# Optimization experiments

Measured on AMD Instinct MI355X. Metric: run time of the kernel, lower is better.

## Reference

```python
import jax, jax.numpy as jnp
import numpy as np

B, T, R, NS = 16, 2048, 256, 4


def setup_inputs() -> dict:
    key = jax.random.key(0)
    ks = jax.random.split(key, 11)
    s = 1.0 / np.sqrt(R)
    inp = {
        "q": jax.random.normal(ks[0], (B, T, R), jnp.float32),
        "k": jax.random.normal(ks[1], (B, T, R), jnp.float32),
        "v": jax.random.normal(ks[2], (B, T, R), jnp.float32),
        "wq": jax.random.uniform(ks[3], (R, R), jnp.float32, -s, s),
        "bq": jax.random.uniform(ks[4], (R,), jnp.float32, -s, s),
        "wk": jax.random.uniform(ks[5], (R, R), jnp.float32, -s, s),
        "bk": jax.random.uniform(ks[6], (R,), jnp.float32, -s, s),
        "wv": jax.random.uniform(ks[7], (NS, R, R), jnp.float32, -s, s),
        "bv": jax.random.uniform(ks[8], (NS, R), jnp.float32, -s, s),
        "wp": jax.random.uniform(ks[9], (R,), jnp.float32, -s, s),
        "bp": jax.random.uniform(ks[10], (), jnp.float32, -s, s),
    }
    return inp


def reference(q, k, v, wq, bq, wk, bk, wv, bv, wp, bp):
    # linear projections (torch Linear: x @ W.T + b)
    qp = q @ wq.T + bq                                   # [B,T,R]
    kp = k @ wk.T + bk                                   # [B,T,R]
    # n_state value projections, stacked on dim 1 -> [B,NS,T,R]
    vs = jnp.einsum('btr,nor->bnto', v, wv) + bv[None, :, None, :]

    # scaled dot-product attention with tril + (score==0 -> -10000) mask quirk
    scale = 1.0 / jnp.sqrt(jnp.asarray(q.shape[-1], qp.dtype))
    score = jnp.einsum('btr,bsr->bts', qp, kp) * scale   # [B,T,T]
    score = jnp.tril(score)
    score = jnp.where(score == 0, jnp.asarray(-10000.0, score.dtype), score)
    attn = jax.nn.softmax(score, axis=-1)                # [B,T,T]

    # batched AV (original does a python loop over batch; same math)
    out = jnp.einsum('bts,bnsr->bntr', attn, vs)         # [B,NS,T,R]

    # similarity loss: 0.5 * sum |cov(proj_score[b])| averaged over batch
    proj = jnp.einsum('bntr,r->bnt', vs, wp) + bp        # [B,NS,T]

    def cov_abs_sum(X):  # X: [NS, T], rows = variables
        Xc = X - X.mean(axis=1, keepdims=True)
        c = (Xc @ Xc.T) / (X.shape[1] - 1)               # [NS,NS]
        return 0.5 * jnp.sum(jnp.abs(c))

    sim_loss = jnp.mean(jax.vmap(cov_abs_sum)(proj))
    return out, sim_loss
```

## Files before the change

### kernel.cpp

```cpp
#include <hip/hip_runtime.h>

#define B_  16
#define T_  2048
#define R_  256
#define NS_ 4

typedef unsigned short u16;
typedef __attribute__((ext_vector_type(8))) __bf16 bf16x8;
typedef __attribute__((ext_vector_type(4))) float f32x4;

__device__ __forceinline__ u16 f2bf(float f){
  union { float f; unsigned u; } x; x.f = f;
  unsigned r = x.u + 0x7FFFu + ((x.u >> 16) & 1u);
  return (u16)(r >> 16);
}
__device__ __forceinline__ float bf2f(u16 h){
  union { unsigned u; float f; } x; x.u = ((unsigned)h) << 16; return x.f;
}

__device__ __forceinline__ void async_cp16(const void* g, void* l){
  __builtin_amdgcn_global_load_lds((__attribute__((address_space(1))) void*)g,
                                   (__attribute__((address_space(3))) void*)l,
                                   16, 0, 0);
}

__global__ __launch_bounds__(256)
void cvt_kernel(const float* __restrict__ src, u16* __restrict__ dst, int n4){
  int i = blockIdx.x*256 + threadIdx.x;
  if (i >= n4) return;
  float4 f = ((const float4*)src)[i];
  ushort4 o;
  o.x = f2bf(f.x); o.y = f2bf(f.y); o.z = f2bf(f.z); o.w = f2bf(f.w);
  ((ushort4*)dst)[i] = o;
}

__global__ __launch_bounds__(256)
void zero_kernel(float* __restrict__ p, int n){
  int i = blockIdx.x*256 + threadIdx.x;
  if (i < n) p[i] = 0.0f;
}

__global__ __launch_bounds__(256)
void pzero_kernel(u16* __restrict__ P){
  int blk = blockIdx.x;
  int b = blk & 15, tT = blk >> 4;
  long long base = (long long)b*T_*T_ + (long long)(tT*256)*T_ + (tT*256 + 128);
  int r = threadIdx.x >> 1, h = threadIdx.x & 1;
  u16* p = P + base + (long long)r*T_ + h*64;
  uint4 z = {0u,0u,0u,0u};
  #pragma unroll
  for (int i=0;i<8;i++) ((uint4*)p)[i] = z;
}

__global__ __launch_bounds__(256, 2)
void gemm_nt_bias(const u16* __restrict__ A, const u16* __restrict__ Bm,
                  u16* __restrict__ C, const float* __restrict__ bias,
                  int lda, int ldb, int ldc, int K,
                  long long sAn, long long sBb, long long sCz,
                  int sBiasN, int biasMode)
{
  __shared__ __align__(16) u16 As[128*32];
  __shared__ __align__(16) u16 Bs[128*32];
  int tid = threadIdx.x;
  int lane = tid & 63, wave = tid >> 6;
  int z = blockIdx.z;
  int nIdx = z & 3, bIdx = z >> 2;
  A    += (long long)nIdx * sAn;
  Bm   += (long long)bIdx * sBb;
  C    += (long long)z * sCz;
  bias += (long long)nIdx * sBiasN;
  int mBase = blockIdx.y * 128;
  int nBase = blockIdx.x * 128;
  int wm = (wave >> 1) * 64, wn = (wave & 1) * 64;
  int quad = lane >> 4, lc = lane & 15;

  f32x4 acc[4][4];
  #pragma unroll
  for (int i=0;i<4;i++)
    #pragma unroll
    for (int j=0;j<4;j++) acc[i][j] = (f32x4){0.f,0.f,0.f,0.f};

  for (int k0=0; k0<K; k0+=32){
    #pragma unroll
    for (int r=0;r<2;r++){
      int c = r*256 + tid;
      int row = c >> 2, col = (c & 3)*8;
      async_cp16(A  + (long long)(mBase+row)*lda + k0 + col, (void*)(As + (r*256 + wave*64)*8));
      async_cp16(Bm + (long long)(nBase+row)*ldb + k0 + col, (void*)(Bs + (r*256 + wave*64)*8));
    }
    __syncthreads();
    bf16x8 af[4], bfr[4];
    #pragma unroll
    for (int i=0;i<4;i++){
      af[i]  = *(const bf16x8*)(As + (wm + i*16 + lc)*32 + quad*8);
      bfr[i] = *(const bf16x8*)(Bs + (wn + i*16 + lc)*32 + quad*8);
    }
    #pragma unroll
    for (int i=0;i<4;i++)
      #pragma unroll
      for (int j=0;j<4;j++)
        acc[i][j] = __builtin_amdgcn_mfma_f32_16x16x32_bf16(af[i], bfr[j], acc[i][j], 0,0,0);
    __syncthreads();
  }
  #pragma unroll
  for (int i=0;i<4;i++){
    #pragma unroll
    for (int j=0;j<4;j++){
      int colG = nBase + wn + j*16 + lc;
      float bc = (biasMode==0) ? bias[colG] : 0.0f;
      #pragma unroll
      for (int e=0;e<4;e++){
        int rowG = mBase + wm + i*16 + quad*4 + e;
        float val = acc[i][j][e] + ((biasMode==0) ? bc : bias[rowG]);
        C[(long long)rowG*ldc + colG] = f2bf(val);
      }
    }
  }
}

__global__ __launch_bounds__(256, 4)
void attn_kernel(const u16* __restrict__ qp, const u16* __restrict__ kp,
                 u16* __restrict__ P, float* __restrict__ lsum)
{
  __shared__ __align__(16) u16 Qs[64*32];
  __shared__ __align__(16) u16 Ks[128*32];
  int tid = threadIdx.x, lane = tid & 63, wave = tid >> 6;
  int b = blockIdx.y;
  int f = blockIdx.x;
  int t64 = 31;
  while (f >= (t64 >> 1) + 1){ f -= (t64 >> 1) + 1; t64--; }
  int sT = f;
  int tBase = t64 * 64;
  const u16* Q  = qp + ((long long)b*T_ + tBase) * R_;
  const u16* Kt = kp + (long long)b*T_*R_ + (long long)sT*128*R_;
  u16* Pb = P + (long long)b*T_*T_;
  const float scale = 0.0625f;
  int quad = lane >> 4, lc = lane & 15;
  int rowLoc = wave*16 + quad*4;

  f32x4 acc[8];
  #pragma unroll
  for (int j=0;j<8;j++) acc[j] = (f32x4){0.f,0.f,0.f,0.f};

  for (int k0=0;k0<R_;k0+=32){
    {
      int row = tid >> 2, col = (tid & 3)*8;
      async_cp16(Q + (long long)row*R_ + k0 + col, (void*)(Qs + (wave*64)*8));
    }
    #pragma unroll
    for (int r=0;r<2;r++){
      int c = r*256 + tid;
      int row = c >> 2, col = (c & 3)*8;
      async_cp16(Kt + (long long)row*R_ + k0 + col, (void*)(Ks + (r*256 + wave*64)*8));
    }
    __syncthreads();
    bf16x8 aq = *(const bf16x8*)(Qs + (wave*16 + lc)*32 + quad*8);
    #pragma unroll
    for (int j=0;j<8;j++){
      bf16x8 bk = *(const bf16x8*)(Ks + (j*16 + lc)*32 + quad*8);
      acc[j] = __builtin_amdgcn_mfma_f32_16x16x32_bf16(aq, bk, acc[j], 0,0,0);
    }
    __syncthreads();
  }

  int sCol0 = sT*128 + lc;
  #pragma unroll
  for (int e=0;e<4;e++){
    int t = tBase + rowLoc + e;
    long long ro = (long long)t * T_;
    float rs = 0.0f;
    #pragma unroll
    for (int j=0;j<8;j++){
      float v = acc[j][e]*scale;
      int s = sCol0 + j*16;
      if (s > t || v == 0.0f) v = -10000.0f;
      float p = __expf(v);
      rs += p;
      Pb[ro + s] = f2bf(p);
    }
    #pragma unroll
    for (int off=1; off<16; off<<=1)
      rs += __shfl_xor(rs, off, 64);
    if (lc == 0)
      atomicAdd(&lsum[b*T_ + t], rs);
  }
}

#define MF(A,Bx,C) __builtin_amdgcn_mfma_f32_16x16x32_bf16(A,Bx,C,0,0,0)
#define VM8 asm volatile("s_waitcnt vmcnt(8)" ::: "memory")
#define VM6 asm volatile("s_waitcnt vmcnt(6)" ::: "memory")
#define VM4 asm volatile("s_waitcnt vmcnt(4)" ::: "memory")
#define VM0 asm volatile("s_waitcnt vmcnt(0)" ::: "memory")

#define STAGE_A(KT,KH) do { \
  const u16* sp_ = aG + (int)((KT)*64 + (KH)*32); \
  u16* dp_ = (u16*)lds + (((KT)&1)*16384 + (KH)*8192 + wave*512); \
  async_cp16(sp_ + stOff, dp_); \
  async_cp16(sp_ + stOff + 128*2048, dp_ + 4096); \
} while(0)
#define STAGE_B(KT,KH) do { \
  const u16* sp_ = bG + (int)((KT)*64 + (KH)*32); \
  u16* dp_ = (u16*)lds + (32768 + ((KT)&1)*16384 + (KH)*8192 + wave*512); \
  async_cp16(sp_ + stOff, dp_); \
  async_cp16(sp_ + stOff + 4096*... , dp_); \
} while(0)
#undef STAGE_B
#define STAGE_B(KT,KH) do { \
  const u16* sp_ = bG + (int)((KT)*64 + (KH)*32); \
  u16* dp_ = (u16*)lds + (32768 + ((KT)&1)*16384 + (KH)*8192 + wave*512); \
  async_cp16(sp_ + stOff, dp_); \
  async_cp16(sp_ + stOff + 128*2048, dp_ + 4096); \
} while(0)

#define LDA_F(BUF,KH,CU,TI) (*(const bf16x8*)(&lds[(BUF)*16384 + (KH)*8192 + (rbA + (CU)*64 + (TI)*16)*32 + qSw]))
#define LDB_F(BUF,KH,JJ)    (*(const bf16x8*)(&lds[32768 + (BUF)*16384 + (KH)*8192 + (rbB + (JJ)*16)*32 + qSw]))

#define RD_A(D0,D1,D2,D3,BUF,KH,CU) do { \
  D0 = LDA_F(BUF,KH,CU,0); D1 = LDA_F(BUF,KH,CU,1); \
  D2 = LDA_F(BUF,KH,CU,2); D3 = LDA_F(BUF,KH,CU,3); } while(0)
#define RD_B(D0,D1,D2,D3,BUF,KH) do { \
  D0 = LDB_F(BUF,KH,0); D1 = LDB_F(BUF,KH,1); \
  D2 = LDB_F(BUF,KH,2); D3 = LDB_F(BUF,KH,3); } while(0)

#define PH(CU,A0,A1,A2,A3,Q0,Q1,Q2,Q3,...) do { \
  asm volatile("s_waitcnt lgkmcnt(0)" ::: "memory"); \
  __builtin_amdgcn_sched_barrier(0); \
  __builtin_amdgcn_s_setprio(1); \
  acc[(CU)*4+0][0]=MF(A0,Q0,acc[(CU)*4+0][0]); \
  acc[(CU)*4+0][1]=MF(A0,Q1,acc[(CU)*4+0][1]); \
  acc[(CU)*4+0][2]=MF(A0,Q2,acc[(CU)*4+0][2]); \
  acc[(CU)*4+0][3]=MF(A0,Q3,acc[(CU)*4+0][3]); \
  acc[(CU)*4+1][0]=MF(A1,Q0,acc[(CU)*4+1][0]); \
  acc[(CU)*4+1][1]=MF(A1,Q1,acc[(CU)*4+1][1]); \
  acc[(CU)*4+1][2]=MF(A1,Q2,acc[(CU)*4+1][2]); \
  acc[(CU)*4+1][3]=MF(A1,Q3,acc[(CU)*4+1][3]); \
  acc[(CU)*4+2][0]=MF(A2,Q0,acc[(CU)*4+2][0]); \
  acc[(CU)*4+2][1]=MF(A2,Q1,acc[(CU)*4+2][1]); \
  acc[(CU)*4+2][2]=MF(A2,Q2,acc[(CU)*4+2][2]); \
  acc[(CU)*4+2][3]=MF(A2,Q3,acc[(CU)*4+2][3]); \
  acc[(CU)*4+3][0]=MF(A3,Q0,acc[(CU)*4+3][0]); \
  acc[(CU)*4+3][1]=MF(A3,Q1,acc[(CU)*4+3][1]); \
  acc[(CU)*4+3][2]=MF(A3,Q2,acc[(CU)*4+3][2]); \
  acc[(CU)*4+3][3]=MF(A3,Q3,acc[(CU)*4+3][3]); \
  __builtin_amdgcn_s_setprio(0); \
  __VA_ARGS__ \
  asm volatile("" ::: "memory"); \
  __builtin_amdgcn_s_barrier(); \
} while(0)

__global__ __launch_bounds__(512, 2)
void pv_kernel(const u16* __restrict__ P, const u16* __restrict__ VT,
               const float* __restrict__ lsum, float* __restrict__ out)
{
  __shared__ __align__(16) u16 lds[65536];
  int tid = threadIdx.x, lane = tid & 63, wave = tid >> 6;
  int f = blockIdx.x;
  int xcd = f & 7, s = f >> 3;
  int g = xcd + 8*(s >> 2);
  int jIdx = s & 3;
  int b = g & 15;
  int tT = 7 - (g >> 4);
  int t0abs = tT * 256;
  int nIt = 2*(tT + 1);

  const u16* aG = P  + (long long)b*T_*T_ + (long long)t0abs*T_;
  const u16* bG = VT + (long long)b*1024*T_ + (long long)(jIdx*256)*T_;

  int stRow = tid >> 2;
  int vSt = (stRow & 3) ^ ((stRow >> 2) & 3);
  int stOff = stRow*2048 + (((tid & 3) ^ vSt) << 3);

  int quad = lane >> 4, lc = lane & 15;
  int wm = wave >> 2, wn = wave & 3;
  int vlc = (lc & 3) ^ ((lc >> 2) & 3);
  int qSw = ((quad ^ vlc) << 3);
  int rbA = wm*128 + lc;
  int rbB = wn*64 + lc;

  f32x4 acc[8][4];
  #pragma unroll
  for (int i=0;i<8;i++)
    #pragma unroll
    for (int j=0;j<4;j++) acc[i][j] = (f32x4){0.f,0.f,0.f,0.f};
  bf16x8 fA0,fA1,fA2,fA3, gA0,gA1,gA2,gA3;
  bf16x8 bX0,bX1,bX2,bX3, bY0,bY1,bY2,bY3;

  STAGE_A(0,0); STAGE_B(0,0);
  STAGE_A(0,1); STAGE_B(0,1);
  STAGE_A(1,0); STAGE_B(1,0);
  VM8;
  __builtin_amdgcn_s_barrier();
  RD_A(fA0,fA1,fA2,fA3, 0,0,0);
  RD_B(bX0,bX1,bX2,bX3, 0,0);

  for (int j = 0; j < nIt-1; ++j){
    int k1 = 2*j+1, k2 = 2*j+2, k3 = 2*j+3;
    PH(0, fA0,fA1,fA2,fA3, bX0,bX1,bX2,bX3,
       RD_A(gA0,gA1,gA2,gA3, 0,0,1); STAGE_A(k1,1); VM6; );
    PH(1, gA0,gA1,gA2,gA3, bX0,bX1,bX2,bX3,
       STAGE_B(k1,1);
       RD_A(fA0,fA1,fA2,fA3, 0,1,0); RD_B(bY0,bY1,bY2,bY3, 0,1); );
    PH(0, fA0,fA1,fA2,fA3, bY0,bY1,bY2,bY3,
       RD_A(gA0,gA1,gA2,gA3, 0,1,1); STAGE_A(k2,0); VM6; );
    PH(1, gA0,gA1,gA2,gA3, bY0,bY1,bY2,bY3,
       STAGE_B(k2,0);
       RD_A(fA0,fA1,fA2,fA3, 1,0,0); RD_B(bX0,bX1,bX2,bX3, 1,0); );
    PH(0, fA0,fA1,fA2,fA3, bX0,bX1,bX2,bX3,
       RD_A(gA0,gA1,gA2,gA3, 1,0,1); STAGE_A(k2,1); VM6; );
    PH(1, gA0,gA1,gA2,gA3, bX0,bX1,bX2,bX3,
       STAGE_B(k2,1);
       RD_A(fA0,fA1,fA2,fA3, 1,1,0); RD_B(bY0,bY1,bY2,bY3, 1,1); );
    PH(0, fA0,fA1,fA2,fA3, bY0,bY1,bY2,bY3,
       RD_A(gA0,gA1,gA2,gA3, 1,1,1); STAGE_A(k3,0); VM6; );
    PH(1, gA0,gA1,gA2,gA3, bY0,bY1,bY2,bY3,
       STAGE_B(k3,0);
       RD_A(fA0,fA1,fA2,fA3, 0,0,0); RD_B(bX0,bX1,bX2,bX3, 0,0); );
  }
  {
    int kL = 2*nIt - 1;
    PH(0, fA0,fA1,fA2,fA3, bX0,bX1,bX2,bX3,
       RD_A(gA0,gA1,gA2,gA3, 0,0,1); STAGE_A(kL,1); VM6; );
    PH(1, gA0,gA1,gA2,gA3, bX0,bX1,bX2,bX3,
       STAGE_B(kL,1);
       RD_A(fA0,fA1,fA2,fA3, 0,1,0); RD_B(bY0,bY1,bY2,bY3, 0,1); );
    PH(0, fA0,fA1,fA2,fA3, bY0,bY1,bY2,bY3,
       RD_A(gA0,gA1,gA2,gA3, 0,1,1); VM4; );
    PH(1, gA0,gA1,gA2,gA3, bY0,bY1,bY2,bY3,
       RD_A(fA0,fA1,fA2,fA3, 1,0,0); RD_B(bX0,bX1,bX2,bX3, 1,0); );
    PH(0, fA0,fA1,fA2,fA3, bX0,bX1,bX2,bX3,
       RD_A(gA0,gA1,gA2,gA3, 1,0,1); VM0; );
    PH(1, gA0,gA1,gA2,gA3, bX0,bX1,bX2,bX3,
       RD_A(fA0,fA1,fA2,fA3, 1,1,0); RD_B(bY0,bY1,bY2,bY3, 1,1); );
    PH(0, fA0,fA1,fA2,fA3, bY0,bY1,bY2,bY3,
       RD_A(gA0,gA1,gA2,gA3, 1,1,1); );
    PH(1, gA0,gA1,gA2,gA3, bY0,bY1,bY2,bY3, );
  }

  const float* lrow = lsum + b*T_;
  #pragma unroll
  for (int i=0;i<8;i++){
    float rl[4];
    #pragma unroll
    for (int e=0;e<4;e++)
      rl[e] = __builtin_amdgcn_rcpf(lrow[t0abs + wm*128 + i*16 + quad*4 + e]);
    #pragma unroll
    for (int j2=0;j2<4;j2++){
      int rcol = wn*64 + j2*16 + lc;
      #pragma unroll
      for (int e=0;e<4;e++){
        int t = t0abs + wm*128 + i*16 + quad*4 + e;
        out[(((long long)b*NS_ + jIdx)*T_ + t)*R_ + rcol] = acc[i][j2][e] * rl[e];
      }
    }
  }
}

__global__ __launch_bounds__(256)
void proj_kernel(const u16* __restrict__ VT, const float* __restrict__ wp,
                 const float* __restrict__ bp, float* __restrict__ proj){
  int gid = blockIdx.x*256 + threadIdx.x;
  int bn = gid >> 11, t = gid & 2047;
  const u16* base = VT + (long long)bn*R_*T_ + t;
  float acc = bp[0];
  #pragma unroll 8
  for (int o=0;o<R_;o++)
    acc = fmaf(bf2f(base[(long long)o*T_]), wp[o], acc);
  proj[gid] = acc;
}

__global__ __launch_bounds__(256)
void loss_batch_kernel(const float* __restrict__ proj, float* __restrict__ partial){
  __shared__ float red[4][14];
  int tid = threadIdx.x, lane = tid & 63, wave = tid >> 6;
  int b = blockIdx.x;
  const float* pb = proj + b*NS_*T_;
  float s[14];
  #pragma unroll
  for (int kk=0;kk<14;kk++) s[kk]=0.0f;
  for (int t=tid; t<T_; t+=256){
    float x0 = pb[0*T_+t], x1 = pb[1*T_+t], x2 = pb[2*T_+t], x3 = pb[3*T_+t];
    s[0]+=x0; s[1]+=x1; s[2]+=x2; s[3]+=x3;
    s[4]+=x0*x0; s[5]+=x1*x0; s[6]+=x1*x1; s[7]+=x2*x0; s[8]+=x2*x1;
    s[9]+=x2*x2; s[10]+=x3*x0; s[11]+=x3*x1; s[12]+=x3*x2; s[13]+=x3*x3;
  }
  #pragma unroll
  for (int kk=0;kk<14;kk++){
    #pragma unroll
    for (int off=1; off<64; off<<=1)
      s[kk] += __shfl_xor(s[kk], off, 64);
  }
  if (lane == 0){
    #pragma unroll
    for (int kk=0;kk<14;kk++) red[wave][kk] = s[kk];
  }
  __syncthreads();
  if (tid == 0){
    float tot[14];
    #pragma unroll
    for (int kk=0;kk<14;kk++)
      tot[kk] = red[0][kk] + red[1][kk] + red[2][kk] + red[3][kk];
    const float invT  = 1.0f/(float)T_;
    const float invT1 = 1.0f/(float)(T_-1);
    float csum = 0.0f;
    #pragma unroll
    for (int n=0;n<4;n++){
      #pragma unroll
      for (int m=0;m<=n;m++){
        int id = n*(n+1)/2 + m;
        float c = (tot[4+id] - tot[n]*tot[m]*invT) * invT1;
        csum += (n==m) ? fabsf(c) : 2.0f*fabsf(c);
      }
    }
    partial[b] = 0.5f*csum;
  }
}

__global__ void loss_final_kernel(const float* __restrict__ partial,
                                  float* __restrict__ simOut){
  if (threadIdx.x == 0){
    float sim = 0.0f;
    #pragma unroll
    for (int b=0;b<B_;b++) sim += partial[b];
    simOut[0] = sim * (1.0f/(float)B_);
  }
}

extern "C" void kernel_launch(void* const* d_in, const int* in_sizes, int n_in,
                              void* d_out, int out_size, void* d_ws, size_t ws_size,
                              hipStream_t stream)
{
  const float* q  = (const float*)d_in[0];
  const float* k  = (const float*)d_in[1];
  const float* v  = (const float*)d_in[2];
  const float* wq = (const float*)d_in[3];
  const float* bq = (const float*)d_in[4];
  const float* wk = (const float*)d_in[5];
  const float* bk = (const float*)d_in[6];
  const float* wv = (const float*)d_in[7];
  const float* bv = (const float*)d_in[8];
  const float* wp = (const float*)d_in[9];
  const float* bp = (const float*)d_in[10];
  float* out = (float*)d_out;

  char* ws = (char*)d_ws;
  u16* qbf   = (u16*)(ws + 0);
  u16* kbf   = (u16*)(ws + 16777216);
  u16* vbf   = (u16*)(ws + 33554432);
  u16* wqbf  = (u16*)(ws + 50331648);
  u16* wkbf  = (u16*)(ws + 50462720);
  u16* wvbf  = (u16*)(ws + 50593792);
  u16* qpbf  = (u16*)(ws + 51118080);
  u16* kpbf  = (u16*)(ws + 67895296);
  u16* vtbf  = (u16*)(ws + 84672512);
  u16* pbuf  = (u16*)(ws + 151781376);
  float* prj = (float*)(ws + 285999104);
  float* lpart = (float*)(ws + 0);
  float* lsum  = (float*)(ws + 16777216);

  cvt_kernel<<<8192,256,0,stream>>>(q,  qbf, 2097152);
  cvt_kernel<<<8192,256,0,stream>>>(k,  kbf, 2097152);
  cvt_kernel<<<8192,256,0,stream>>>(v,  vbf, 2097152);
  cvt_kernel<<<64,  256,0,stream>>>(wq, wqbf, 16384);
  cvt_kernel<<<64,  256,0,stream>>>(wk, wkbf, 16384);
  cvt_kernel<<<256, 256,0,stream>>>(wv, wvbf, 65536);

  dim3 gq(2,256,1);
  gemm_nt_bias<<<gq,256,0,stream>>>(qbf, wqbf, qpbf, bq, 256,256,256,256, 0,0,0, 0, 0);
  gemm_nt_bias<<<gq,256,0,stream>>>(kbf, wkbf, kpbf, bk, 256,256,256,256, 0,0,0, 0, 0);
  dim3 gv(16,2,64);
  gemm_nt_bias<<<gv,256,0,stream>>>(wvbf, vbf, vtbf, bv, 256,256,2048,256,
                                    65536LL, 524288LL, 524288LL, 256, 1);

  zero_kernel<<<128,256,0,stream>>>(lsum, 32768);
  pzero_kernel<<<128,256,0,stream>>>(pbuf);
  dim3 ga(272,16,1);
  attn_kernel<<<ga,256,0,stream>>>(qpbf, kpbf, pbuf, lsum);

  pv_kernel<<<512,512,0,stream>>>(pbuf, vtbf, lsum, out);

  proj_kernel<<<512,256,0,stream>>>(vtbf, wp, bp, prj);
  loss_batch_kernel<<<16,256,0,stream>>>(prj, lpart);
  loss_final_kernel<<<1,64,0,stream>>>(lpart, out + 33554432);
}
```

Baseline: 469.8 us.

## Split waves into two roles that issue LDS reads before or after MFMAs

Waves 4-7 (roleB) now issue the next phase's LDS fragment reads and async global-to-LDS staging before their MFMA block, waiting only on a partial lgkmcnt, while waves 0-3 keep the old order of compute first, then loads. The intent is to stagger LDS traffic against MFMA issue across the two wave groups, so the shared memory pipe and the matrix units are busy at the same time instead of in lockstep. It also drops a dead duplicate STAGE_B definition and moves STAGE_B after the register reads in odd phases. The risks are wrong lgkmcnt counts, which could let an MFMA read a fragment that has not arrived, and extra branch divergence at wave level.

```diff
diff --git a/kernel.cpp b/kernel.cpp
--- a/kernel.cpp
+++ b/kernel.cpp
@@ -202,13 +202,6 @@
   const u16* sp_ = bG + (int)((KT)*64 + (KH)*32); \
   u16* dp_ = (u16*)lds + (32768 + ((KT)&1)*16384 + (KH)*8192 + wave*512); \
   async_cp16(sp_ + stOff, dp_); \
-  async_cp16(sp_ + stOff + 4096*... , dp_); \
-} while(0)
-#undef STAGE_B
-#define STAGE_B(KT,KH) do { \
-  const u16* sp_ = bG + (int)((KT)*64 + (KH)*32); \
-  u16* dp_ = (u16*)lds + (32768 + ((KT)&1)*16384 + (KH)*8192 + wave*512); \
-  async_cp16(sp_ + stOff, dp_); \
   async_cp16(sp_ + stOff + 128*2048, dp_ + 4096); \
 } while(0)
 
@@ -222,10 +215,7 @@
   D0 = LDB_F(BUF,KH,0); D1 = LDB_F(BUF,KH,1); \
   D2 = LDB_F(BUF,KH,2); D3 = LDB_F(BUF,KH,3); } while(0)
 
-#define PH(CU,A0,A1,A2,A3,Q0,Q1,Q2,Q3,...) do { \
-  asm volatile("s_waitcnt lgkmcnt(0)" ::: "memory"); \
-  __builtin_amdgcn_sched_barrier(0); \
-  __builtin_amdgcn_s_setprio(1); \
+#define MFMAS(CU,A0,A1,A2,A3,Q0,Q1,Q2,Q3) do { \
   acc[(CU)*4+0][0]=MF(A0,Q0,acc[(CU)*4+0][0]); \
   acc[(CU)*4+0][1]=MF(A0,Q1,acc[(CU)*4+0][1]); \
   acc[(CU)*4+0][2]=MF(A0,Q2,acc[(CU)*4+0][2]); \
@@ -242,8 +232,24 @@
   acc[(CU)*4+3][1]=MF(A3,Q1,acc[(CU)*4+3][1]); \
   acc[(CU)*4+3][2]=MF(A3,Q2,acc[(CU)*4+3][2]); \
   acc[(CU)*4+3][3]=MF(A3,Q3,acc[(CU)*4+3][3]); \
-  __builtin_amdgcn_s_setprio(0); \
-  __VA_ARGS__ \
+} while(0)
+
+#define PH(CU,A0,A1,A2,A3,Q0,Q1,Q2,Q3,NLG,...) do { \
+  if (roleB) { \
+    __VA_ARGS__ \
+    asm volatile("s_waitcnt lgkmcnt(" #NLG ")" ::: "memory"); \
+    __builtin_amdgcn_sched_barrier(0); \
+    __builtin_amdgcn_s_setprio(1); \
+    MFMAS(CU,A0,A1,A2,A3,Q0,Q1,Q2,Q3); \
+    __builtin_amdgcn_s_setprio(0); \
+  } else { \
+    asm volatile("s_waitcnt lgkmcnt(0)" ::: "memory"); \
+    __builtin_amdgcn_sched_barrier(0); \
+    __builtin_amdgcn_s_setprio(1); \
+    MFMAS(CU,A0,A1,A2,A3,Q0,Q1,Q2,Q3); \
+    __builtin_amdgcn_s_setprio(0); \
+    __VA_ARGS__ \
+  } \
   asm volatile("" ::: "memory"); \
   __builtin_amdgcn_s_barrier(); \
 } while(0)
@@ -254,6 +260,7 @@
 {
   __shared__ __align__(16) u16 lds[65536];
   int tid = threadIdx.x, lane = tid & 63, wave = tid >> 6;
+  const int roleB = wave >> 2;
   int f = blockIdx.x;
   int xcd = f & 7, s = f >> 3;
   int g = xcd + 8*(s >> 2);
@@ -295,45 +302,45 @@
 
   for (int j = 0; j < nIt-1; ++j){
     int k1 = 2*j+1, k2 = 2*j+2, k3 = 2*j+3;
-    PH(0, fA0,fA1,fA2,fA3, bX0,bX1,bX2,bX3,
+    PH(0, fA0,fA1,fA2,fA3, bX0,bX1,bX2,bX3, 4,
        RD_A(gA0,gA1,gA2,gA3, 0,0,1); STAGE_A(k1,1); VM6; );
-    PH(1, gA0,gA1,gA2,gA3, bX0,bX1,bX2,bX3,
-       STAGE_B(k1,1);
-       RD_A(fA0,fA1,fA2,fA3, 0,1,0); RD_B(bY0,bY1,bY2,bY3, 0,1); );
-    PH(0, fA0,fA1,fA2,fA3, bY0,bY1,bY2,bY3,
+    PH(1, gA0,gA1,gA2,gA3, bX0,bX1,bX2,bX3, 8,
+       RD_A(fA0,fA1,fA2,fA3, 0,1,0); RD_B(bY0,bY1,bY2,bY3, 0,1);
+       STAGE_B(k1,1); );
+    PH(0, fA0,fA1,fA2,fA3, bY0,bY1,bY2,bY3, 4,
        RD_A(gA0,gA1,gA2,gA3, 0,1,1); STAGE_A(k2,0); VM6; );
-    PH(1, gA0,gA1,gA2,gA3, bY0,bY1,bY2,bY3,
-       STAGE_B(k2,0);
-       RD_A(fA0,fA1,fA2,fA3, 1,0,0); RD_B(bX0,bX1,bX2,bX3, 1,0); );
-    PH(0, fA0,fA1,fA2,fA3, bX0,bX1,bX2,bX3,
+    PH(1, gA0,gA1,gA2,gA3, bY0,bY1,bY2,bY3, 8,
+       RD_A(fA0,fA1,fA2,fA3, 1,0,0); RD_B(bX0,bX1,bX2,bX3, 1,0);
+       STAGE_B(k2,0); );
+    PH(0, fA0,fA1,fA2,fA3, bX0,bX1,bX2,bX3, 4,
        RD_A(gA0,gA1,gA2,gA3, 1,0,1); STAGE_A(k2,1); VM6; );
-    PH(1, gA0,gA1,gA2,gA3, bX0,bX1,bX2,bX3,
-       STAGE_B(k2,1);
-       RD_A(fA0,fA1,fA2,fA3, 1,1,0); RD_B(bY0,bY1,bY2,bY3, 1,1); );
-    PH(0, fA0,fA1,fA2,fA3, bY0,bY1,bY2,bY3,
+    PH(1, gA0,gA1,gA2,gA3, bX0,bX1,bX2,bX3, 8,
+       RD_A(fA0,fA1,fA2,fA3, 1,1,0); RD_B(bY0,bY1,bY2,bY3, 1,1);
+       STAGE_B(k2,1); );
+    PH(0, fA0,fA1,fA2,fA3, bY0,bY1,bY2,bY3, 4,
        RD_A(gA0,gA1,gA2,gA3, 1,1,1); STAGE_A(k3,0); VM6; );
-    PH(1, gA0,gA1,gA2,gA3, bY0,bY1,bY2,bY3,
-       STAGE_B(k3,0);
-       RD_A(fA0,fA1,fA2,fA3, 0,0,0); RD_B(bX0,bX1,bX2,bX3, 0,0); );
+    PH(1, gA0,gA1,gA2,gA3, bY0,bY1,bY2,bY3, 8,
+       RD_A(fA0,fA1,fA2,fA3, 0,0,0); RD_B(bX0,bX1,bX2,bX3, 0,0);
+       STAGE_B(k3,0); );
   }
   {
     int kL = 2*nIt - 1;
-    PH(0, fA0,fA1,fA2,fA3, bX0,bX1,bX2,bX3,
+    PH(0, fA0,fA1,fA2,fA3, bX0,bX1,bX2,bX3, 4,
        RD_A(gA0,gA1,gA2,gA3, 0,0,1); STAGE_A(kL,1); VM6; );
-    PH(1, gA0,gA1,gA2,gA3, bX0,bX1,bX2,bX3,
-       STAGE_B(kL,1);
-       RD_A(fA0,fA1,fA2,fA3, 0,1,0); RD_B(bY0,bY1,bY2,bY3, 0,1); );
-    PH(0, fA0,fA1,fA2,fA3, bY0,bY1,bY2,bY3,
+    PH(1, gA0,gA1,gA2,gA3, bX0,bX1,bX2,bX3, 8,
+       RD_A(fA0,fA1,fA2,fA3, 0,1,0); RD_B(bY0,bY1,bY2,bY3, 0,1);
+       STAGE_B(kL,1); );
+    PH(0, fA0,fA1,fA2,fA3, bY0,bY1,bY2,bY3, 4,
        RD_A(gA0,gA1,gA2,gA3, 0,1,1); VM4; );
-    PH(1, gA0,gA1,gA2,gA3, bY0,bY1,bY2,bY3,
+    PH(1, gA0,gA1,gA2,gA3, bY0,bY1,bY2,bY3, 8,
        RD_A(fA0,fA1,fA2,fA3, 1,0,0); RD_B(bX0,bX1,bX2,bX3, 1,0); );
-    PH(0, fA0,fA1,fA2,fA3, bX0,bX1,bX2,bX3,
+    PH(0, fA0,fA1,fA2,fA3, bX0,bX1,bX2,bX3, 4,
        RD_A(gA0,gA1,gA2,gA3, 1,0,1); VM0; );
-    PH(1, gA0,gA1,gA2,gA3, bX0,bX1,bX2,bX3,
+    PH(1, gA0,gA1,gA2,gA3, bX0,bX1,bX2,bX3, 8,
        RD_A(fA0,fA1,fA2,fA3, 1,1,0); RD_B(bY0,bY1,bY2,bY3, 1,1); );
-    PH(0, fA0,fA1,fA2,fA3, bY0,bY1,bY2,bY3,
+    PH(0, fA0,fA1,fA2,fA3, bY0,bY1,bY2,bY3, 4,
        RD_A(gA0,gA1,gA2,gA3, 1,1,1); );
-    PH(1, gA0,gA1,gA2,gA3, bY0,bY1,bY2,bY3, );
+    PH(1, gA0,gA1,gA2,gA3, bY0,bY1,bY2,bY3, 0, );
   }
 
   const float* lrow = lsum + b*T_;
```

Result: slower. 815.0 us (+73.5%).
